# Kernel tuning notes

Measured on AMD Instinct MI355X. Metric: run time of the kernel, lower is better.

Reference implementation:

```python
import jax, jax.numpy as jnp
import numpy as np

SIG = 10
C = 0.0
STD = 1.0
N_ATOMS = 21
N_TRAIN = 8192
DESC = N_ATOMS * (N_ATOMS - 1) // 2  # 210
M = 64


def setup_inputs() -> dict:
    key = jax.random.key(0)
    k1, k2, k3 = jax.random.split(key, 3)
    Rs = jax.random.normal(k1, (M, N_ATOMS, 3), dtype=jnp.float32)
    xs_train = jax.random.uniform(k2, (N_TRAIN, DESC), dtype=jnp.float32)
    Jx_alphas = jax.random.normal(k3, (N_TRAIN, DESC), dtype=jnp.float32)
    return {"Rs": Rs, "xs_train": xs_train, "Jx_alphas": Jx_alphas}


def reference(Rs, xs_train, Jx_alphas):
    sig = SIG
    q = np.sqrt(5.0) / sig
    n = N_ATOMS
    # pairwise atom displacements / distances: [M, n, n, 3], [M, n, n]
    diffs = Rs[:, :, None, :] - Rs[:, None, :, :]
    dists = jnp.linalg.norm(diffs, axis=-1)
    eye = jnp.eye(n, dtype=bool)
    dists = jnp.where(eye, jnp.inf, dists)  # kill diagonal
    i, j = np.tril_indices(n, k=-1)
    xs = 1.0 / dists[:, i, j]                       # [M, D] inverse-distance descriptor
    x_diffs = q * xs[:, None, :] - q * xs_train     # [M, T, D]
    x_dists = jnp.linalg.norm(x_diffs, axis=-1)     # [M, T]
    exp_xs = (5.0 / (3.0 * sig ** 2)) * jnp.exp(-x_dists)
    dot = jnp.einsum('mtd,td->mt', x_diffs, Jx_alphas)
    exp_xs_1 = exp_xs * (1.0 + x_dists)
    F1s_x = jnp.einsum('mt,mtd->md', exp_xs * dot, x_diffs)  # [M, D]
    F2s_x = exp_xs_1 @ Jx_alphas                              # [M, D]
    Fs_x = (F1s_x - F2s_x) * STD
    # expand_tril: scatter D lower-tri values to symmetric [M, n, n], zero diag
    full = jnp.zeros((Fs_x.shape[0], n, n), dtype=Fs_x.dtype)
    full = full.at[:, i, j].set(Fs_x).at[:, j, i].set(Fs_x)
    Fs = jnp.einsum('mab,mabc->mac', full / dists ** 3, diffs)  # diag: 0/inf -> 0
    Es = jnp.sum(exp_xs_1 * dot, axis=-1) / q
    Es = C + Es * STD
    return Es, Fs
```

## Files before the change

### kernel.cpp

```cpp
#include <hip/hip_runtime.h>
#include <math.h>

#define NA   21
#define NM   64
#define ND   210
#define DP   224
#define NT   8192
#define NCH  28
#define KS2  32

#define QC 0.22360679774997896f
#define KE 0.016666666666666666f

typedef short bf8 __attribute__((ext_vector_type(8)));
typedef float f4  __attribute__((ext_vector_type(4)));

#define O_XFT  1835008u
#define O_JFT  2752512u
#define O_W1   3670016u
#define O_E1   3932160u
#define O_AF   4194304u
#define O_QG   4201472u
#define O_NX   4232192u
#define O_PB   4261056u
#define O_ESP  5178560u
#define O_WAP  5211328u

__device__ __forceinline__ unsigned short f2bf(float f) {
    unsigned u = __float_as_uint(f);
    u += 0x7fffu + ((u >> 16) & 1u);
    return (unsigned short)(u >> 16);
}
__device__ __forceinline__ float bf2f(unsigned short h) {
    return __uint_as_float((unsigned)h << 16);
}

__device__ __forceinline__ void d_to_ij(int d, int& i, int& j) {
    int ii = (int)((1.0f + sqrtf(1.0f + 8.0f * (float)d)) * 0.5f);
    while (ii * (ii - 1) / 2 > d) --ii;
    while ((ii + 1) * ii / 2 <= d) ++ii;
    i = ii;
    j = d - ii * (ii - 1) / 2;
}

__global__ __launch_bounds__(256) void k_geom(
    const float* __restrict__ Rs, unsigned short* __restrict__ Af,
    float* __restrict__ qxsG, float* __restrict__ nx) {
    const int m = blockIdx.x, tid = threadIdx.x;
    __shared__ float R[NA * 3];
    __shared__ float red[256];
    if (tid < NA * 3) R[tid] = Rs[m * NA * 3 + tid];
    __syncthreads();
    float local = 0.0f;
    if (tid < DP) {
        float vr = 0.0f;
        unsigned short hv = 0;
        if (tid < ND) {
            int i, j; d_to_ij(tid, i, j);
            float dx = R[i * 3] - R[j * 3];
            float dy = R[i * 3 + 1] - R[j * 3 + 1];
            float dz = R[i * 3 + 2] - R[j * 3 + 2];
            float v = QC / sqrtf(dx * dx + dy * dy + dz * dz);
            hv = f2bf(v);
            vr = bf2f(hv);
        }
        Af[(((m >> 4) * NCH + (tid >> 3)) * 16 + (m & 15)) * 8 + (tid & 7)] = hv;
        qxsG[(tid >> 2) * 256 + m * 4 + (tid & 3)] = vr;
        local = vr * vr;
    }
    red[tid] = local;
    __syncthreads();
    for (int s = 128; s > 0; s >>= 1) {
        if (tid < s) red[tid] += red[tid + s];
        __syncthreads();
    }
    if (tid == 0) nx[m] = red[0];
}

__global__ __launch_bounds__(256) void k_s1p(
    const float* __restrict__ xs, const float* __restrict__ Jx,
    const unsigned short* __restrict__ Af, const float* __restrict__ nxg,
    unsigned short* __restrict__ XfT, unsigned short* __restrict__ JfT,
    unsigned short* __restrict__ w1f, unsigned short* __restrict__ e1f,
    float* __restrict__ EsPart, float* __restrict__ WaPart) {
    const int b = blockIdx.x, tid = threadIdx.x;
    const int lane = tid & 63;
    const int w = tid >> 6;
    const int col = lane & 15, quad = lane >> 4;

    __shared__ unsigned short xJh[2 * 16 * DP];
    __shared__ float Dw[64][17];
    __shared__ float De[64][17];
    __shared__ float ntL[16], cjL[16];
    char* xB = (char*)xJh;

    const unsigned short* ap = Af + ((size_t)(w * NCH + quad) * 16 + col) * 8;
    bf8 af[7];
#pragma unroll
    for (int kc = 0; kc < 7; ++kc) af[kc] = *(const bf8*)(ap + kc * 512);
    float nxv[4];
#pragma unroll
    for (int r = 0; r < 4; ++r) nxv[r] = nxg[w * 16 + quad * 4 + r];

    if (tid < 224) {
        const int arr = tid / 112, rem = tid - arr * 112;
        const int t = rem / 7, k2 = rem - t * 7;
        *(unsigned*)(xB + arr * 7168 +
                     (((unsigned)(t * 448 + 420 + k2 * 4)) ^ ((unsigned)((t & 7) << 4)))) = 0u;
    }
    const float2* sx = (const float2*)(xs + (size_t)b * 16 * ND);
    const float2* sj = (const float2*)(Jx + (size_t)b * 16 * ND);
#pragma unroll
    for (int k = 0; k < 7; ++k) {
        const int p = k * 256 + tid;
        if (p < 1680) {
            const float2 vx = sx[p];
            const float2 vj = sj[p];
            const int t = p / 105;
            const unsigned bo = ((unsigned)(4 * p + 28 * t)) ^ ((unsigned)((t & 7) << 4));
            *(unsigned*)(xB + bo) =
                (unsigned)f2bf(QC * vx.x) | ((unsigned)f2bf(QC * vx.y) << 16);
            *(unsigned*)(xB + 7168 + bo) =
                (unsigned)f2bf(vj.x) | ((unsigned)f2bf(vj.y) << 16);
        }
    }
    __syncthreads();

    const unsigned base0 = (unsigned)(col * 448 + quad * 16);
    const unsigned swc = (unsigned)((col & 7) << 4);
    bf8 bx[2], bj[2];
    bx[0] = *(const bf8*)(xB + (base0 ^ swc));
    bj[0] = *(const bf8*)(xB + 7168 + (base0 ^ swc));
    bx[1] = *(const bf8*)(xB + ((base0 + 64) ^ swc));
    bj[1] = *(const bf8*)(xB + 7168 + ((base0 + 64) ^ swc));
    f4 c1 = {0.f, 0.f, 0.f, 0.f};
    f4 c2 = {0.f, 0.f, 0.f, 0.f};
#pragma unroll
    for (int kc = 0; kc < 7; ++kc) {
        const int s = kc & 1;
        c1 = __builtin_amdgcn_mfma_f32_16x16x32_bf16(af[kc], bx[s], c1, 0, 0, 0);
        c2 = __builtin_amdgcn_mfma_f32_16x16x32_bf16(af[kc], bj[s], c2, 0, 0, 0);
        if (kc < 5) {
            bx[s] = *(const bf8*)(xB + ((base0 + (kc + 2) * 64) ^ swc));
            bj[s] = *(const bf8*)(xB + 7168 + ((base0 + (kc + 2) * 64) ^ swc));
        }
    }

    {
        const int tt = tid >> 4, l = tid & 15;
        const unsigned swt = (unsigned)((tt & 7) << 4);
        float sn = 0.0f, sc2 = 0.0f;
#pragma unroll
        for (int c = l; c < DP; c += 16) {
            const unsigned off = ((unsigned)(tt * 448 + 2 * c)) ^ swt;
            const float x = bf2f(*(const unsigned short*)(xB + off));
            const float jv = bf2f(*(const unsigned short*)(xB + 7168 + off));
            sn = fmaf(x, x, sn);
            sc2 = fmaf(x, jv, sc2);
        }
#pragma unroll
        for (int o = 1; o < 16; o <<= 1) {
            sn += __shfl_xor(sn, o);
            sc2 += __shfl_xor(sc2, o);
        }
        if (l == 0) { ntL[tt] = sn; cjL[tt] = sc2; }
    }
    __syncthreads();

    const float ntv = ntL[col], cjv = cjL[col];
    float esA[4], wlA[4];
#pragma unroll
    for (int r = 0; r < 4; ++r) {
        const int m = w * 16 + quad * 4 + r;
        float sq = fmaxf(nxv[r] - 2.0f * c1[r] + ntv, 0.0f);
        float xd = sqrtf(sq);
        float e = KE * expf(-xd);
        float dotv = c2[r] - cjv;
        float wv = e * dotv;
        float ev = e * (1.0f + xd);
        Dw[m][col] = wv;
        De[m][col] = ev;
        esA[r] = ev * dotv;
        wlA[r] = wv;
    }
    __syncthreads();

    {
        const int aidx = tid >> 7;
        const int c = tid & 127;
        const int mtile = c >> 5, tql = (c >> 4) & 1, colm = c & 15;
        const float* srcD = aidx ? &De[0][0] : &Dw[0][0];
        unsigned short* dst = aidx ? e1f : w1f;
        const int m = mtile * 16 + colm;
        union { unsigned short us[8]; uint4 v; } u;
#pragma unroll
        for (int i = 0; i < 8; ++i) u.us[i] = f2bf(srcD[m * 17 + tql * 8 + i]);
        const size_t off = ((size_t)(mtile * 1024 + b * 2 + tql) * 16 + colm) * 8;
        *(uint4*)(dst + off) = u.v;
    }
#pragma unroll
    for (int k = 0; k < 4; ++k) {
        const int idx = k * 256 + tid;
        if (idx < 896) {
            const int arr = idx / 448;
            const int rem = idx - arr * 448;
            const int dtile = rem >> 5;
            const int rem2 = rem & 31;
            const int tql = rem2 >> 4, cc = rem2 & 15;
            const int dbyte = 2 * (dtile * 16 + cc);
            union { unsigned short us[8]; uint4 v; } u;
#pragma unroll
            for (int i = 0; i < 8; ++i) {
                const int t = tql * 8 + i;
                const unsigned off =
                    ((unsigned)(t * 448 + dbyte)) ^ ((unsigned)((t & 7) << 4));
                u.us[i] = *(const unsigned short*)(xB + arr * 7168 + off);
            }
            const size_t o2 = ((size_t)(dtile * 1024 + b * 2 + tql) * 16 + cc) * 8;
            *(uint4*)((arr ? JfT : XfT) + o2) = u.v;
        }
    }
#pragma unroll
    for (int r = 0; r < 4; ++r) {
        float e = esA[r], wl = wlA[r];
#pragma unroll
        for (int o = 1; o < 16; o <<= 1) {
            e += __shfl_xor(e, o);
            wl += __shfl_xor(wl, o);
        }
        if (col == 0) {
            const int m = w * 16 + quad * 4 + r;
            EsPart[(size_t)m * 512 + b] = e;
            WaPart[(size_t)m * 512 + b] = wl;
        }
    }
}

__global__ __launch_bounds__(256) void k_stage2(
    const unsigned short* __restrict__ w1f, const unsigned short* __restrict__ e1f,
    const unsigned short* __restrict__ XfT, const unsigned short* __restrict__ JfT,
    float* __restrict__ Pbuf) {
    const int tid = threadIdx.x;
    const int lane = tid & 63;
    const int w = tid >> 6;
    const int col = lane & 15, quad = lane >> 4;
    const int dt = blockIdx.x;
    const int by = blockIdx.y;

    const unsigned short* awp = w1f + ((size_t)(w * 1024 + by * 32 + quad) * 16 + col) * 8;
    const unsigned short* aep = e1f + ((size_t)(w * 1024 + by * 32 + quad) * 16 + col) * 8;
    const unsigned short* bxp = XfT + ((size_t)(dt * 1024 + by * 32 + quad) * 16 + col) * 8;
    const unsigned short* bjp = JfT + ((size_t)(dt * 1024 + by * 32 + quad) * 16 + col) * 8;

    bf8 aw[2], ae[2], bx[2], bj[2];
    aw[0] = *(const bf8*)awp;         ae[0] = *(const bf8*)aep;
    bx[0] = *(const bf8*)bxp;         bj[0] = *(const bf8*)bjp;
    aw[1] = *(const bf8*)(awp + 512); ae[1] = *(const bf8*)(aep + 512);
    bx[1] = *(const bf8*)(bxp + 512); bj[1] = *(const bf8*)(bjp + 512);

    f4 dA = {0.f, 0.f, 0.f, 0.f};
    f4 dB = {0.f, 0.f, 0.f, 0.f};
#pragma unroll
    for (int kk = 0; kk < 8; ++kk) {
        const int s = kk & 1;
        dA = __builtin_amdgcn_mfma_f32_16x16x32_bf16(aw[s], bx[s], dA, 0, 0, 0);
        dB = __builtin_amdgcn_mfma_f32_16x16x32_bf16(ae[s], bj[s], dB, 0, 0, 0);
        if (kk < 6) {
            aw[s] = *(const bf8*)(awp + (kk + 2) * 512);
            ae[s] = *(const bf8*)(aep + (kk + 2) * 512);
            bx[s] = *(const bf8*)(bxp + (kk + 2) * 512);
            bj[s] = *(const bf8*)(bjp + (kk + 2) * 512);
        }
    }
#pragma unroll
    for (int r = 0; r < 4; ++r) {
        const int m = w * 16 + quad * 4 + r;
        Pbuf[((size_t)(m * KS2 + by)) * DP + dt * 16 + col] = dA[r] + dB[r];
    }
}

__global__ void k_final(const float* __restrict__ Rs, const float* __restrict__ qxsG,
                        const float* __restrict__ Pbuf, const float* __restrict__ EsPart,
                        const float* __restrict__ WaPart, float* __restrict__ out) {
    int m = blockIdx.x, tid = threadIdx.x;
    __shared__ float R[NA * 3];
    __shared__ float Ff[NA][NA];
    __shared__ float redE[256];
    __shared__ float redW[256];
    __shared__ float ABs[DP];
    if (tid < NA * 3) R[tid] = Rs[m * NA * 3 + tid];
    if (tid < NA) Ff[tid][tid] = 0.0f;
    if (tid < DP) {
        const float* p0 = Pbuf + (size_t)m * KS2 * DP + tid;
        float s1 = 0.0f;
#pragma unroll
        for (int ks = 0; ks < KS2; ++ks) s1 += p0[ks * DP];
        ABs[tid] = s1;
    }
    {
        const float2 ep = ((const float2*)(EsPart + (size_t)m * 512))[tid];
        const float2 wp = ((const float2*)(WaPart + (size_t)m * 512))[tid];
        redE[tid] = ep.x + ep.y;
        redW[tid] = wp.x + wp.y;
    }
    __syncthreads();
    for (int s = 128; s > 0; s >>= 1) {
        if (tid < s) {
            redE[tid] += redE[tid + s];
            redW[tid] += redW[tid + s];
        }
        __syncthreads();
    }
    const float Wa = redW[0];
    if (tid < ND) {
        int i, j; d_to_ij(tid, i, j);
        float dx = R[i * 3] - R[j * 3];
        float dy = R[i * 3 + 1] - R[j * 3 + 1];
        float dz = R[i * 3 + 2] - R[j * 3 + 2];
        float dist2 = dx * dx + dy * dy + dz * dz;
        float fsx = qxsG[(tid >> 2) * 256 + m * 4 + (tid & 3)] * Wa - ABs[tid];
        float f = fsx / (dist2 * sqrtf(dist2));
        Ff[i][j] = f;
        Ff[j][i] = f;
    }
    __syncthreads();
    if (tid < NA * 3) {
        int a = tid / 3, c = tid % 3;
        float s = 0.0f;
        for (int b = 0; b < NA; ++b) {
            if (b == a) continue;
            s += Ff[a][b] * (R[a * 3 + c] - R[b * 3 + c]);
        }
        out[NM + m * NA * 3 + tid] = s;
    }
    if (tid == 0) out[m] = redE[0] / QC;
}

extern "C" void kernel_launch(void* const* d_in, const int* in_sizes, int n_in,
                              void* d_out, int out_size, void* d_ws, size_t ws_size,
                              hipStream_t stream) {
    const float* Rs = (const float*)d_in[0];
    const float* xs_train = (const float*)d_in[1];
    const float* Jx_alphas = (const float*)d_in[2];
    float* out = (float*)d_out;
    float* ws = (float*)d_ws;

    unsigned short* XfT = (unsigned short*)(ws + O_XFT);
    unsigned short* JfT = (unsigned short*)(ws + O_JFT);
    unsigned short* w1f = (unsigned short*)(ws + O_W1);
    unsigned short* e1f = (unsigned short*)(ws + O_E1);
    unsigned short* Af  = (unsigned short*)(ws + O_AF);
    float* qxsG   = ws + O_QG;
    float* nx     = ws + O_NX;
    float* Pbuf   = ws + O_PB;
    float* EsPart = ws + O_ESP;
    float* WaPart = ws + O_WAP;

    k_geom<<<NM, 256, 0, stream>>>(Rs, Af, qxsG, nx);
    k_s1p<<<512, 256, 0, stream>>>(xs_train, Jx_alphas, Af, nx, XfT, JfT,
                                   w1f, e1f, EsPart, WaPart);
    k_stage2<<<dim3(14, KS2), 256, 0, stream>>>(w1f, e1f, XfT, JfT, Pbuf);
    k_final<<<NM, 256, 0, stream>>>(Rs, qxsG, Pbuf, EsPart, WaPart, out);
}
```

Measured before the change: 85.27 us.

## Fuse stage-2 GEMM into stage-1 kernel using LDS-resident train tiles

Merges the stage-1 distance/weight kernel and the stage-2 reduction GEMM into one kernel. Each 512-thread block handles 32 training rows and computes the second MFMA product straight from the bf16 x/J tiles and weights already in shared memory. This drops the global round-trip through XfT/JfT/w1f/e1f and one kernel launch. In exchange the per-block partials grow from 32 to 256 slices per molecule, so the final kernel's reduction over Pbuf reads eight times more data, and the stage-2 operand loads become scalar LDS gathers.

```diff
diff --git a/kernel.cpp b/kernel.cpp
--- a/kernel.cpp
+++ b/kernel.cpp
@@ -7,7 +7,6 @@
 #define DP   224
 #define NT   8192
 #define NCH  28
-#define KS2  32
 
 #define QC 0.22360679774997896f
 #define KE 0.016666666666666666f
@@ -15,16 +14,12 @@
 typedef short bf8 __attribute__((ext_vector_type(8)));
 typedef float f4  __attribute__((ext_vector_type(4)));
 
-#define O_XFT  1835008u
-#define O_JFT  2752512u
-#define O_W1   3670016u
-#define O_E1   3932160u
-#define O_AF   4194304u
-#define O_QG   4201472u
-#define O_NX   4232192u
-#define O_PB   4261056u
-#define O_ESP  5178560u
-#define O_WAP  5211328u
+#define O_AF   0u
+#define O_QG   7168u
+#define O_NX   21504u
+#define O_ESP  21568u
+#define O_WAP  54336u
+#define O_PB   87104u
 
 __device__ __forceinline__ unsigned short f2bf(float f) {
     unsigned u = __float_as_uint(f);
@@ -77,62 +72,62 @@
     if (tid == 0) nx[m] = red[0];
 }
 
-__global__ __launch_bounds__(256) void k_s1p(
+__global__ __launch_bounds__(512) void k_s1p2(
     const float* __restrict__ xs, const float* __restrict__ Jx,
     const unsigned short* __restrict__ Af, const float* __restrict__ nxg,
-    unsigned short* __restrict__ XfT, unsigned short* __restrict__ JfT,
-    unsigned short* __restrict__ w1f, unsigned short* __restrict__ e1f,
-    float* __restrict__ EsPart, float* __restrict__ WaPart) {
+    float* __restrict__ EsPart, float* __restrict__ WaPart,
+    float* __restrict__ Pbuf) {
     const int b = blockIdx.x, tid = threadIdx.x;
     const int lane = tid & 63;
-    const int w = tid >> 6;
+    const int wave = tid >> 6;
+    const int mtile = wave & 3, sub = wave >> 2;
     const int col = lane & 15, quad = lane >> 4;
 
-    __shared__ unsigned short xJh[2 * 16 * DP];
-    __shared__ float Dw[64][17];
-    __shared__ float De[64][17];
-    __shared__ float ntL[16], cjL[16];
+    __shared__ unsigned short xJh[2 * 32 * DP];
+    __shared__ unsigned short Dwh[64][33];
+    __shared__ unsigned short Deh[64][33];
+    __shared__ float ntL[32], cjL[32];
     char* xB = (char*)xJh;
 
-    const unsigned short* ap = Af + ((size_t)(w * NCH + quad) * 16 + col) * 8;
+    const unsigned short* ap = Af + ((size_t)(mtile * NCH + quad) * 16 + col) * 8;
     bf8 af[7];
 #pragma unroll
     for (int kc = 0; kc < 7; ++kc) af[kc] = *(const bf8*)(ap + kc * 512);
     float nxv[4];
 #pragma unroll
-    for (int r = 0; r < 4; ++r) nxv[r] = nxg[w * 16 + quad * 4 + r];
-
-    if (tid < 224) {
-        const int arr = tid / 112, rem = tid - arr * 112;
+    for (int r = 0; r < 4; ++r) nxv[r] = nxg[mtile * 16 + quad * 4 + r];
+
+    if (tid < 448) {
+        const int arr = tid / 224, rem = tid - arr * 224;
         const int t = rem / 7, k2 = rem - t * 7;
-        *(unsigned*)(xB + arr * 7168 +
+        *(unsigned*)(xB + arr * 14336 +
                      (((unsigned)(t * 448 + 420 + k2 * 4)) ^ ((unsigned)((t & 7) << 4)))) = 0u;
     }
-    const float2* sx = (const float2*)(xs + (size_t)b * 16 * ND);
-    const float2* sj = (const float2*)(Jx + (size_t)b * 16 * ND);
+    const float2* sx = (const float2*)(xs + (size_t)b * 32 * ND);
+    const float2* sj = (const float2*)(Jx + (size_t)b * 32 * ND);
 #pragma unroll
     for (int k = 0; k < 7; ++k) {
-        const int p = k * 256 + tid;
-        if (p < 1680) {
+        const int p = k * 512 + tid;
+        if (p < 3360) {
             const float2 vx = sx[p];
             const float2 vj = sj[p];
             const int t = p / 105;
             const unsigned bo = ((unsigned)(4 * p + 28 * t)) ^ ((unsigned)((t & 7) << 4));
             *(unsigned*)(xB + bo) =
                 (unsigned)f2bf(QC * vx.x) | ((unsigned)f2bf(QC * vx.y) << 16);
-            *(unsigned*)(xB + 7168 + bo) =
+            *(unsigned*)(xB + 14336 + bo) =
                 (unsigned)f2bf(vj.x) | ((unsigned)f2bf(vj.y) << 16);
         }
     }
     __syncthreads();
 
-    const unsigned base0 = (unsigned)(col * 448 + quad * 16);
+    const unsigned base0 = (unsigned)((sub * 16 + col) * 448 + quad * 16);
     const unsigned swc = (unsigned)((col & 7) << 4);
     bf8 bx[2], bj[2];
     bx[0] = *(const bf8*)(xB + (base0 ^ swc));
-    bj[0] = *(const bf8*)(xB + 7168 + (base0 ^ swc));
+    bj[0] = *(const bf8*)(xB + 14336 + (base0 ^ swc));
     bx[1] = *(const bf8*)(xB + ((base0 + 64) ^ swc));
-    bj[1] = *(const bf8*)(xB + 7168 + ((base0 + 64) ^ swc));
+    bj[1] = *(const bf8*)(xB + 14336 + ((base0 + 64) ^ swc));
     f4 c1 = {0.f, 0.f, 0.f, 0.f};
     f4 c2 = {0.f, 0.f, 0.f, 0.f};
 #pragma unroll
@@ -142,7 +137,7 @@
         c2 = __builtin_amdgcn_mfma_f32_16x16x32_bf16(af[kc], bj[s], c2, 0, 0, 0);
         if (kc < 5) {
             bx[s] = *(const bf8*)(xB + ((base0 + (kc + 2) * 64) ^ swc));
-            bj[s] = *(const bf8*)(xB + 7168 + ((base0 + (kc + 2) * 64) ^ swc));
+            bj[s] = *(const bf8*)(xB + 14336 + ((base0 + (kc + 2) * 64) ^ swc));
         }
     }
 
@@ -154,7 +149,7 @@
         for (int c = l; c < DP; c += 16) {
             const unsigned off = ((unsigned)(tt * 448 + 2 * c)) ^ swt;
             const float x = bf2f(*(const unsigned short*)(xB + off));
-            const float jv = bf2f(*(const unsigned short*)(xB + 7168 + off));
+            const float jv = bf2f(*(const unsigned short*)(xB + 14336 + off));
             sn = fmaf(x, x, sn);
             sc2 = fmaf(x, jv, sc2);
         }
@@ -167,58 +162,22 @@
     }
     __syncthreads();
 
-    const float ntv = ntL[col], cjv = cjL[col];
+    const int tloc = sub * 16 + col;
+    const float ntv = ntL[tloc], cjv = cjL[tloc];
     float esA[4], wlA[4];
 #pragma unroll
     for (int r = 0; r < 4; ++r) {
-        const int m = w * 16 + quad * 4 + r;
+        const int m = mtile * 16 + quad * 4 + r;
         float sq = fmaxf(nxv[r] - 2.0f * c1[r] + ntv, 0.0f);
         float xd = sqrtf(sq);
         float e = KE * expf(-xd);
         float dotv = c2[r] - cjv;
         float wv = e * dotv;
         float ev = e * (1.0f + xd);
-        Dw[m][col] = wv;
-        De[m][col] = ev;
+        Dwh[m][tloc] = f2bf(wv);
+        Deh[m][tloc] = f2bf(ev);
         esA[r] = ev * dotv;
         wlA[r] = wv;
-    }
-    __syncthreads();
-
-    {
-        const int aidx = tid >> 7;
-        const int c = tid & 127;
-        const int mtile = c >> 5, tql = (c >> 4) & 1, colm = c & 15;
-        const float* srcD = aidx ? &De[0][0] : &Dw[0][0];
-        unsigned short* dst = aidx ? e1f : w1f;
-        const int m = mtile * 16 + colm;
-        union { unsigned short us[8]; uint4 v; } u;
-#pragma unroll
-        for (int i = 0; i < 8; ++i) u.us[i] = f2bf(srcD[m * 17 + tql * 8 + i]);
-        const size_t off = ((size_t)(mtile * 1024 + b * 2 + tql) * 16 + colm) * 8;
-        *(uint4*)(dst + off) = u.v;
-    }
-#pragma unroll
-    for (int k = 0; k < 4; ++k) {
-        const int idx = k * 256 + tid;
-        if (idx < 896) {
-            const int arr = idx / 448;
-            const int rem = idx - arr * 448;
-            const int dtile = rem >> 5;
-            const int rem2 = rem & 31;
-            const int tql = rem2 >> 4, cc = rem2 & 15;
-            const int dbyte = 2 * (dtile * 16 + cc);
-            union { unsigned short us[8]; uint4 v; } u;
-#pragma unroll
-            for (int i = 0; i < 8; ++i) {
-                const int t = tql * 8 + i;
-                const unsigned off =
-                    ((unsigned)(t * 448 + dbyte)) ^ ((unsigned)((t & 7) << 4));
-                u.us[i] = *(const unsigned short*)(xB + arr * 7168 + off);
-            }
-            const size_t o2 = ((size_t)(dtile * 1024 + b * 2 + tql) * 16 + cc) * 8;
-            *(uint4*)((arr ? JfT : XfT) + o2) = u.v;
-        }
     }
 #pragma unroll
     for (int r = 0; r < 4; ++r) {
@@ -229,53 +188,40 @@
             wl += __shfl_xor(wl, o);
         }
         if (col == 0) {
-            const int m = w * 16 + quad * 4 + r;
-            EsPart[(size_t)m * 512 + b] = e;
-            WaPart[(size_t)m * 512 + b] = wl;
-        }
-    }
-}
-
-__global__ __launch_bounds__(256) void k_stage2(
-    const unsigned short* __restrict__ w1f, const unsigned short* __restrict__ e1f,
-    const unsigned short* __restrict__ XfT, const unsigned short* __restrict__ JfT,
-    float* __restrict__ Pbuf) {
-    const int tid = threadIdx.x;
-    const int lane = tid & 63;
-    const int w = tid >> 6;
-    const int col = lane & 15, quad = lane >> 4;
-    const int dt = blockIdx.x;
-    const int by = blockIdx.y;
-
-    const unsigned short* awp = w1f + ((size_t)(w * 1024 + by * 32 + quad) * 16 + col) * 8;
-    const unsigned short* aep = e1f + ((size_t)(w * 1024 + by * 32 + quad) * 16 + col) * 8;
-    const unsigned short* bxp = XfT + ((size_t)(dt * 1024 + by * 32 + quad) * 16 + col) * 8;
-    const unsigned short* bjp = JfT + ((size_t)(dt * 1024 + by * 32 + quad) * 16 + col) * 8;
-
-    bf8 aw[2], ae[2], bx[2], bj[2];
-    aw[0] = *(const bf8*)awp;         ae[0] = *(const bf8*)aep;
-    bx[0] = *(const bf8*)bxp;         bj[0] = *(const bf8*)bjp;
-    aw[1] = *(const bf8*)(awp + 512); ae[1] = *(const bf8*)(aep + 512);
-    bx[1] = *(const bf8*)(bxp + 512); bj[1] = *(const bf8*)(bjp + 512);
-
-    f4 dA = {0.f, 0.f, 0.f, 0.f};
-    f4 dB = {0.f, 0.f, 0.f, 0.f};
-#pragma unroll
-    for (int kk = 0; kk < 8; ++kk) {
-        const int s = kk & 1;
-        dA = __builtin_amdgcn_mfma_f32_16x16x32_bf16(aw[s], bx[s], dA, 0, 0, 0);
-        dB = __builtin_amdgcn_mfma_f32_16x16x32_bf16(ae[s], bj[s], dB, 0, 0, 0);
-        if (kk < 6) {
-            aw[s] = *(const bf8*)(awp + (kk + 2) * 512);
-            ae[s] = *(const bf8*)(aep + (kk + 2) * 512);
-            bx[s] = *(const bf8*)(bxp + (kk + 2) * 512);
-            bj[s] = *(const bf8*)(bjp + (kk + 2) * 512);
-        }
-    }
-#pragma unroll
-    for (int r = 0; r < 4; ++r) {
-        const int m = w * 16 + quad * 4 + r;
-        Pbuf[((size_t)(m * KS2 + by)) * DP + dt * 16 + col] = dA[r] + dB[r];
+            const int m = mtile * 16 + quad * 4 + r;
+            EsPart[(size_t)m * 512 + b * 2 + sub] = e;
+            WaPart[(size_t)m * 512 + b * 2 + sub] = wl;
+        }
+    }
+    __syncthreads();
+
+    union { unsigned short us[8]; bf8 v; } uaw, uae;
+#pragma unroll
+    for (int i = 0; i < 8; ++i) {
+        uaw.us[i] = Dwh[mtile * 16 + col][quad * 8 + i];
+        uae.us[i] = Deh[mtile * 16 + col][quad * 8 + i];
+    }
+    const int dt0 = sub * 7;
+#pragma unroll
+    for (int dd = 0; dd < 7; ++dd) {
+        const int dt = dt0 + dd;
+        union { unsigned short us[8]; bf8 v; } ubx, ubj;
+#pragma unroll
+        for (int i = 0; i < 8; ++i) {
+            const int t = quad * 8 + i;
+            const unsigned off =
+                ((unsigned)(t * 448 + 2 * (dt * 16 + col))) ^ ((unsigned)((t & 7) << 4));
+            ubx.us[i] = *(const unsigned short*)(xB + off);
+            ubj.us[i] = *(const unsigned short*)(xB + 14336 + off);
+        }
+        f4 z = {0.f, 0.f, 0.f, 0.f};
+        f4 dA = __builtin_amdgcn_mfma_f32_16x16x32_bf16(uaw.v, ubx.v, z, 0, 0, 0);
+        f4 dB = __builtin_amdgcn_mfma_f32_16x16x32_bf16(uae.v, ubj.v, z, 0, 0, 0);
+#pragma unroll
+        for (int r = 0; r < 4; ++r) {
+            const int m = mtile * 16 + quad * 4 + r;
+            Pbuf[((size_t)(m * 256 + b)) * DP + dt * 16 + col] = dA[r] + dB[r];
+        }
     }
 }
 
@@ -291,11 +237,16 @@
     if (tid < NA * 3) R[tid] = Rs[m * NA * 3 + tid];
     if (tid < NA) Ff[tid][tid] = 0.0f;
     if (tid < DP) {
-        const float* p0 = Pbuf + (size_t)m * KS2 * DP + tid;
-        float s1 = 0.0f;
-#pragma unroll
-        for (int ks = 0; ks < KS2; ++ks) s1 += p0[ks * DP];
-        ABs[tid] = s1;
+        const float* p0 = Pbuf + (size_t)m * 256 * DP + tid;
+        float s0 = 0.0f, s1 = 0.0f, s2 = 0.0f, s3 = 0.0f;
+#pragma unroll
+        for (int bb = 0; bb < 256; bb += 4) {
+            s0 += p0[(bb + 0) * DP];
+            s1 += p0[(bb + 1) * DP];
+            s2 += p0[(bb + 2) * DP];
+            s3 += p0[(bb + 3) * DP];
+        }
+        ABs[tid] = (s0 + s1) + (s2 + s3);
     }
     {
         const float2 ep = ((const float2*)(EsPart + (size_t)m * 512))[tid];
@@ -345,20 +296,15 @@
     float* out = (float*)d_out;
     float* ws = (float*)d_ws;
 
-    unsigned short* XfT = (unsigned short*)(ws + O_XFT);
-    unsigned short* JfT = (unsigned short*)(ws + O_JFT);
-    unsigned short* w1f = (unsigned short*)(ws + O_W1);
-    unsigned short* e1f = (unsigned short*)(ws + O_E1);
-    unsigned short* Af  = (unsigned short*)(ws + O_AF);
+    unsigned short* Af = (unsigned short*)(ws + O_AF);
     float* qxsG   = ws + O_QG;
     float* nx     = ws + O_NX;
-    float* Pbuf   = ws + O_PB;
     float* EsPart = ws + O_ESP;
     float* WaPart = ws + O_WAP;
+    float* Pbuf   = ws + O_PB;
 
     k_geom<<<NM, 256, 0, stream>>>(Rs, Af, qxsG, nx);
-    k_s1p<<<512, 256, 0, stream>>>(xs_train, Jx_alphas, Af, nx, XfT, JfT,
-                                   w1f, e1f, EsPart, WaPart);
-    k_stage2<<<dim3(14, KS2), 256, 0, stream>>>(w1f, e1f, XfT, JfT, Pbuf);
+    k_s1p2<<<256, 512, 0, stream>>>(xs_train, Jx_alphas, Af, nx,
+                                    EsPart, WaPart, Pbuf);
     k_final<<<NM, 256, 0, stream>>>(Rs, qxsG, Pbuf, EsPart, WaPart, out);
 }
```

Result: no change. 85.95 us (+0.8%).
